# Performance work log

Measured on AMD Instinct MI355X. Metric: run time of the kernel, lower is better.

## Reference

```python
import jax, jax.numpy as jnp
import numpy as np

N_NODES = 50000


def _gcn_norm(edge_index, n):
    # add self loops, compute symmetric normalization coefficients
    src = jnp.concatenate([edge_index[0], jnp.arange(n, dtype=edge_index.dtype)])
    dst = jnp.concatenate([edge_index[1], jnp.arange(n, dtype=edge_index.dtype)])
    deg = jax.ops.segment_sum(jnp.ones_like(dst, dtype=jnp.float32), dst, num_segments=n)
    dis = jnp.where(deg > 0, jax.lax.rsqrt(jnp.maximum(deg, 1.0)), 0.0)
    norm = dis[src] * dis[dst]  # [E+n]
    return src, dst, norm


def _gcn_conv(x, W, b, src, dst, norm, n):
    xw = x @ W                      # [n, out]
    msg = xw[src] * norm[:, None]   # gather + scale
    out = jax.ops.segment_sum(msg, dst, num_segments=n)
    return out + b


def setup_inputs() -> dict:
    key = jax.random.key(0)
    ks = jax.random.split(key, 12)
    n, d, h, E, P = N_NODES, 512, 512, 400000, 200000
    sc = lambda fan_in: 1.0 / np.sqrt(fan_in)
    return {
        "x": jax.random.normal(ks[0], (n, d), dtype=jnp.float32),
        "edge_index": jax.random.randint(ks[1], (2, E), 0, n, dtype=jnp.int32),
        "edge_pairs": jax.random.randint(ks[2], (2, P), 0, n, dtype=jnp.int32),
        "W1": jax.random.uniform(ks[3], (d, h), jnp.float32, -sc(d), sc(d)),
        "b1": jnp.zeros((h,), jnp.float32),
        "W2": jax.random.uniform(ks[4], (h, h), jnp.float32, -sc(h), sc(h)),
        "b2": jnp.zeros((h,), jnp.float32),
        "lpW1": jax.random.uniform(ks[5], (2 * h, h), jnp.float32, -sc(2 * h), sc(2 * h)),
        "lpb1": jax.random.uniform(ks[6], (h,), jnp.float32, -sc(2 * h), sc(2 * h)),
        "lpW2": jax.random.uniform(ks[7], (h, 1), jnp.float32, -sc(h), sc(h)),
        "lpb2": jax.random.uniform(ks[8], (1,), jnp.float32, -sc(h), sc(h)),
    }


def reference(x, edge_index, edge_pairs, W1, b1, W2, b2, lpW1, lpb1, lpW2, lpb2):
    n = x.shape[0]
    src, dst, norm = _gcn_norm(edge_index, n)
    # encoder: GCNConv -> relu -> (dropout is identity at inference) -> GCNConv
    z = _gcn_conv(x, W1, b1, src, dst, norm, n)
    z = jax.nn.relu(z)
    z = _gcn_conv(z, W2, b2, src, dst, norm, n)
    # link predictor: gather-concat MLP
    h = jnp.concatenate([z[edge_pairs[0]], z[edge_pairs[1]]], axis=-1)  # [P, 2h]
    h = jax.nn.relu(h @ lpW1 + lpb1)
    logits = (h @ lpW2 + lpb2)[:, 0]
    return jax.nn.sigmoid(logits)
```

## Files before the change

kernel.cpp:

```cpp
#include <hip/hip_runtime.h>
#include <math.h>

#define TPB 256

typedef __attribute__((ext_vector_type(8))) short bf16x8;
typedef __attribute__((ext_vector_type(4))) float f32x4;

__device__ __forceinline__ unsigned cvt_bf(float f) {
    unsigned u = __float_as_uint(f);
    u += 0x7fffu + ((u >> 16) & 1u);
    return u >> 16;
}
__device__ __forceinline__ unsigned pack2(float a, float b) {
    return cvt_bf(a) | (cvt_bf(b) << 16);
}

__device__ __forceinline__ void gload16(const void* g, void* l) {
    __builtin_amdgcn_global_load_lds(
        (const __attribute__((address_space(1))) void*)g,
        (__attribute__((address_space(3))) void*)l, 16, 0, 0);
}


__global__ void k_hist(const int* __restrict__ dst, int* __restrict__ cnt, int E) {
    int e = blockIdx.x * TPB + threadIdx.x;
    if (e < E) atomicAdd(&cnt[dst[e]], 1);
}

__global__ __launch_bounds__(256)
void k_scan1(const int* __restrict__ cnt, int* __restrict__ incl,
             int* __restrict__ bsum, int n) {
    __shared__ int sh[256];
    const int t = threadIdx.x;
    const int i = blockIdx.x * 256 + t;
    int v = (i < n) ? cnt[i] : 0;
    sh[t] = v;
    __syncthreads();
#pragma unroll
    for (int d = 1; d < 256; d <<= 1) {
        int u = (t >= d) ? sh[t - d] : 0;
        __syncthreads();
        sh[t] += u;
        __syncthreads();
    }
    if (i < n) incl[i] = sh[t];
    if (t == 255) bsum[blockIdx.x] = sh[255];
}

__global__ __launch_bounds__(256)
void k_scan2(int* __restrict__ bsum, int* __restrict__ boff,
             int* __restrict__ row_start, int n, int nb) {
    __shared__ int sh[256];
    const int t = threadIdx.x;
    int v = (t < nb) ? bsum[t] : 0;
    sh[t] = v;
    __syncthreads();
#pragma unroll
    for (int d = 1; d < 256; d <<= 1) {
        int u = (t >= d) ? sh[t - d] : 0;
        __syncthreads();
        sh[t] += u;
        __syncthreads();
    }
    if (t < nb) boff[t] = sh[t] - v;
    if (t == nb - 1) row_start[n] = sh[t];
}

__global__ void k_scan3(const int* __restrict__ cnt, const int* __restrict__ incl,
                        const int* __restrict__ boff, int* __restrict__ row_start,
                        int* __restrict__ cursor, float* __restrict__ dis, int n) {
    int i = blockIdx.x * TPB + threadIdx.x;
    if (i >= n) return;
    int c = cnt[i];
    int ex = boff[i >> 8] + incl[i] - c;
    row_start[i] = ex;
    cursor[i] = ex;
    dis[i] = rsqrtf((float)c + 1.0f);
}

__global__ void k_fill_csr(const int* __restrict__ src, const int* __restrict__ dst,
                           const float* __restrict__ dis, int* __restrict__ cursor,
                           int* __restrict__ csr_src, float* __restrict__ csr_nrm, int E) {
    int e = blockIdx.x * TPB + threadIdx.x;
    if (e >= E) return;
    int s = src[e], d = dst[e];
    int pos = atomicAdd(&cursor[d], 1);
    csr_src[pos] = s;
    csr_nrm[pos] = dis[s] * dis[d];
}


__global__ void k_f2bf(const float* __restrict__ in, unsigned short* __restrict__ out, int total8) {
    int i = blockIdx.x * TPB + threadIdx.x;
    if (i >= total8) return;
    float4 f0 = *(const float4*)(in + (size_t)i * 8);
    float4 f1 = *(const float4*)(in + (size_t)i * 8 + 4);
    uint4 o;
    o.x = pack2(f0.x, f0.y); o.y = pack2(f0.z, f0.w);
    o.z = pack2(f1.x, f1.y); o.w = pack2(f1.z, f1.w);
    *(uint4*)(out + (size_t)i * 8) = o;
}

__global__ void k_cvtT(const float* __restrict__ in, unsigned short* __restrict__ out, int K, int N) {
    int id = blockIdx.x * TPB + threadIdx.x;
    if (id >= K * N) return;
    int k = id / N, nn = id % N;
    out[(size_t)nn * K + k] = (unsigned short)cvt_bf(in[id]);
}

__global__ void k_cvtT_lp(const float* __restrict__ in, unsigned short* __restrict__ out) {
    int id = blockIdx.x * TPB + threadIdx.x;
    if (id >= 1024 * 512) return;
    int j = id >> 9, k = id & 511;
    float v = (j < 512) ? in[(size_t)k * 512 + j] : in[(size_t)(512 + k) * 512 + (j - 512)];
    out[id] = (unsigned short)cvt_bf(v);
}

__global__ __launch_bounds__(256)
void k_bias_lp(const float* __restrict__ lpW1, const float* __restrict__ b2,
               const float* __restrict__ lpb1, float* __restrict__ bias_big) {
    const int j = blockIdx.x * 4 + (threadIdx.x >> 6);
    if (j >= 1024) return;
    const int lane = threadIdx.x & 63;
    const int col = (j < 512) ? j : (j - 512);
    const int ro = (j < 512) ? 0 : 512;
    float s = 0.f;
#pragma unroll
    for (int it = 0; it < 8; ++it) {
        int k = lane + it * 64;
        s = fmaf(b2[k], lpW1[(size_t)(ro + k) * 512 + col], s);
    }
    s += __shfl_xor(s, 1, 64);
    s += __shfl_xor(s, 2, 64);
    s += __shfl_xor(s, 4, 64);
    s += __shfl_xor(s, 8, 64);
    s += __shfl_xor(s, 16, 64);
    s += __shfl_xor(s, 32, 64);
    if (lane == 0) bias_big[j] = s + ((j < 512) ? lpb1[j] : 0.f);
}


__global__ __launch_bounds__(256)
void k_agg_bf(const unsigned short* __restrict__ xin, const int* __restrict__ row_start,
              const int* __restrict__ csr_src, const float* __restrict__ csr_nrm,
              const float* __restrict__ dis, unsigned short* __restrict__ out, int n) {
    const int v = (blockIdx.x * TPB + threadIdx.x) >> 6;
    if (v >= n) return;
    const int lane = threadIdx.x & 63;
    const uint4* base = (const uint4*)xin;

    float d = dis[v]; float d2 = d * d;
    float acc[8];
    {
        uint4 u = base[(size_t)v * 64 + lane];
        acc[0] = d2 * __uint_as_float(u.x << 16);
        acc[1] = d2 * __uint_as_float(u.x & 0xffff0000u);
        acc[2] = d2 * __uint_as_float(u.y << 16);
        acc[3] = d2 * __uint_as_float(u.y & 0xffff0000u);
        acc[4] = d2 * __uint_as_float(u.z << 16);
        acc[5] = d2 * __uint_as_float(u.z & 0xffff0000u);
        acc[6] = d2 * __uint_as_float(u.w << 16);
        acc[7] = d2 * __uint_as_float(u.w & 0xffff0000u);
    }
    const int beg = row_start[v], end = row_start[v + 1];
    for (int j = beg; j < end; ++j) {
        int s = csr_src[j];
        float r = csr_nrm[j];
        uint4 u = base[(size_t)s * 64 + lane];
        acc[0] = fmaf(__uint_as_float(u.x << 16), r, acc[0]);
        acc[1] = fmaf(__uint_as_float(u.x & 0xffff0000u), r, acc[1]);
        acc[2] = fmaf(__uint_as_float(u.y << 16), r, acc[2]);
        acc[3] = fmaf(__uint_as_float(u.y & 0xffff0000u), r, acc[3]);
        acc[4] = fmaf(__uint_as_float(u.z << 16), r, acc[4]);
        acc[5] = fmaf(__uint_as_float(u.z & 0xffff0000u), r, acc[5]);
        acc[6] = fmaf(__uint_as_float(u.w << 16), r, acc[6]);
        acc[7] = fmaf(__uint_as_float(u.w & 0xffff0000u), r, acc[7]);
    }
    uint4 o;
    o.x = pack2(acc[0], acc[1]); o.y = pack2(acc[2], acc[3]);
    o.z = pack2(acc[4], acc[5]); o.w = pack2(acc[6], acc[7]);
    ((uint4*)out)[(size_t)v * 64 + lane] = o;
}


__global__ __launch_bounds__(256)
void k_gemm_bf(const unsigned short* __restrict__ A, const unsigned short* __restrict__ Bt,
               const float* __restrict__ bias, unsigned short* __restrict__ C,
               int M, int K, int N, int do_relu, int nbx) {
    const int lin = blockIdx.x;
    const int xcd = lin & 7, seq = lin >> 3;
    const int rowt = xcd + 8 * (seq / nbx);
    const int colt = seq % nbx;
    const int m0 = rowt * 128;
    if (m0 >= M + 127) return;
    const int n0 = colt * 128;

    __shared__ __align__(16) char Asl[128 * 64];
    __shared__ __align__(16) char Bsl[128 * 64];
    const int t = threadIdx.x;
    const int wid = t >> 6, l = t & 63;
    const int wr = (wid >> 1) * 64, wc = (wid & 1) * 64;
    const int lrow = l & 15, g = l >> 4;

    const int srow = (l >> 2);
    const int cb_src = ((l & 3) * 16) ^ ((srow & 3) << 4);
    const int r0 = wid * 32 + srow, r1 = r0 + 16;
    const size_t rowA0 = (size_t)min(m0 + r0, M - 1) * K * 2;
    const size_t rowA1 = (size_t)min(m0 + r1, M - 1) * K * 2;
    const size_t rowB0 = (size_t)(n0 + r0) * K * 2;
    const size_t rowB1 = (size_t)(n0 + r1) * K * 2;
    const char* Ab = (const char*)A;
    const char* Bb = (const char*)Bt;
    char* ldsA0 = Asl + (wid * 32) * 64;
    char* ldsA1 = ldsA0 + 16 * 64;
    char* ldsB0 = Bsl + (wid * 32) * 64;
    char* ldsB1 = ldsB0 + 16 * 64;

    f32x4 acc[4][4] = {};
    for (int k0 = 0; k0 < K; k0 += 32) {
        const size_t koff = (size_t)k0 * 2 + cb_src;
        gload16(Ab + rowA0 + koff, ldsA0);
        gload16(Ab + rowA1 + koff, ldsA1);
        gload16(Bb + rowB0 + koff, ldsB0);
        gload16(Bb + rowB1 + koff, ldsB1);
        __syncthreads();
        bf16x8 af[4], bfr[4];
#pragma unroll
        for (int i = 0; i < 4; ++i)
            af[i] = *(const bf16x8*)(Asl + (wr + i * 16 + lrow) * 64 + ((g * 16) ^ ((lrow & 3) << 4)));
#pragma unroll
        for (int j = 0; j < 4; ++j)
            bfr[j] = *(const bf16x8*)(Bsl + (wc + j * 16 + lrow) * 64 + ((g * 16) ^ ((lrow & 3) << 4)));
#pragma unroll
        for (int i = 0; i < 4; ++i)
#pragma unroll
            for (int j = 0; j < 4; ++j)
                acc[i][j] = __builtin_amdgcn_mfma_f32_16x16x32_bf16(af[i], bfr[j], acc[i][j], 0, 0, 0);
        __syncthreads();
    }
    float bv[4];
#pragma unroll
    for (int j = 0; j < 4; ++j) bv[j] = bias[n0 + wc + j * 16 + lrow];
#pragma unroll
    for (int i = 0; i < 4; ++i) {
        const int rb = m0 + wr + i * 16 + g * 4;
#pragma unroll
        for (int e = 0; e < 4; ++e) {
            const int row = rb + e;
            if (row < M) {
#pragma unroll
                for (int j = 0; j < 4; ++j) {
                    float vv = acc[i][j][e] + bv[j];
                    if (do_relu) vv = fmaxf(vv, 0.f);
                    C[(size_t)row * N + n0 + wc + j * 16 + lrow] = (unsigned short)cvt_bf(vv);
                }
            }
        }
    }
}


__global__ __launch_bounds__(256)
void k_pair(const unsigned short* __restrict__ uv, const int* __restrict__ pair, int P,
            const float* __restrict__ w2, const float* __restrict__ lpb2,
            float* __restrict__ out) {
    const int idx = (blockIdx.x * TPB + threadIdx.x) >> 6;
    if (idx >= P) return;
    const int lane = threadIdx.x & 63;
    const int p0n = pair[idx], p1n = pair[P + idx];
    const uint4 a = *(const uint4*)(uv + (size_t)p0n * 1024 + lane * 8);
    const uint4 b = *(const uint4*)(uv + (size_t)p1n * 1024 + 512 + lane * 8);
    const float4 w0 = *(const float4*)(w2 + lane * 8);
    const float4 w1 = *(const float4*)(w2 + lane * 8 + 4);
    const unsigned ua[4] = {a.x, a.y, a.z, a.w};
    const unsigned ub[4] = {b.x, b.y, b.z, b.w};
    const float wv[8] = {w0.x, w0.y, w0.z, w0.w, w1.x, w1.y, w1.z, w1.w};
    float s = 0.f;
#pragma unroll
    for (int q = 0; q < 4; ++q) {
        float h0 = __uint_as_float(ua[q] << 16) + __uint_as_float(ub[q] << 16);
        float h1 = __uint_as_float(ua[q] & 0xffff0000u) + __uint_as_float(ub[q] & 0xffff0000u);
        s = fmaf(fmaxf(h0, 0.f), wv[2 * q], s);
        s = fmaf(fmaxf(h1, 0.f), wv[2 * q + 1], s);
    }
    s += __shfl_xor(s, 1, 64);
    s += __shfl_xor(s, 2, 64);
    s += __shfl_xor(s, 4, 64);
    s += __shfl_xor(s, 8, 64);
    s += __shfl_xor(s, 16, 64);
    s += __shfl_xor(s, 32, 64);
    if (lane == 0) out[idx] = 1.0f / (1.0f + expf(-(s + lpb2[0])));
}


extern "C" void kernel_launch(void* const* d_in, const int* in_sizes, int n_in,
                              void* d_out, int out_size, void* d_ws, size_t ws_size,
                              hipStream_t stream) {
    const float* x    = (const float*)d_in[0];
    const int*   ei   = (const int*)d_in[1];
    const int*   ep   = (const int*)d_in[2];
    const float* W1   = (const float*)d_in[3];
    const float* b1   = (const float*)d_in[4];
    const float* W2   = (const float*)d_in[5];
    const float* b2   = (const float*)d_in[6];
    const float* lpW1 = (const float*)d_in[7];
    const float* lpb1 = (const float*)d_in[8];
    const float* lpW2 = (const float*)d_in[9];
    const float* lpb2 = (const float*)d_in[10];

    const int n = in_sizes[0] / 512;
    const int E = in_sizes[1] / 2;
    const int P = in_sizes[2] / 2;
    const int* src = ei;
    const int* dst = ei + E;

    char* w = (char*)d_ws;
    size_t off = 0;
    auto alloc = [&](size_t bytes) {
        void* p = w + off;
        off = (off + bytes + 255) & ~(size_t)255;
        return p;
    };
    int*   cnt       = (int*)alloc((size_t)n * 4);
    int*   incl      = (int*)alloc((size_t)n * 4);
    int*   bsum      = (int*)alloc((size_t)256 * 4);
    int*   boff      = (int*)alloc((size_t)256 * 4);
    int*   row_start = (int*)alloc((size_t)(n + 1) * 4);
    int*   cursor    = (int*)alloc((size_t)n * 4);
    int*   csr_src   = (int*)alloc((size_t)E * 4);
    float* csr_nrm   = (float*)alloc((size_t)E * 4);
    float* dis       = (float*)alloc((size_t)n * 4);
    unsigned short* w1t    = (unsigned short*)alloc((size_t)512 * 512 * 2);
    unsigned short* w2bf   = (unsigned short*)alloc((size_t)512 * 512 * 2);
    unsigned short* lpw1t  = (unsigned short*)alloc((size_t)1024 * 512 * 2);
    unsigned short* wfT    = (unsigned short*)alloc((size_t)1024 * 512 * 2);
    float* bias_big  = (float*)alloc((size_t)1024 * 4);
    float* zerob     = (float*)alloc((size_t)1024 * 4);
    unsigned short* bufA = (unsigned short*)alloc((size_t)n * 512 * 2);
    unsigned short* bufB = (unsigned short*)alloc((size_t)n * 512 * 2);
    unsigned short* uv   = (unsigned short*)alloc((size_t)n * 1024 * 2);

    dim3 blk(TPB);
    const int nb_n = (n + TPB - 1) / TPB;
    const int nb_E = (E + TPB - 1) / TPB;
    const int nb_scan = (n + 255) / 256;

    hipMemsetAsync(cnt, 0, (size_t)n * 4, stream);
    hipMemsetAsync(zerob, 0, (size_t)1024 * 4, stream);
    k_hist<<<nb_E, blk, 0, stream>>>(dst, cnt, E);
    k_scan1<<<nb_scan, 256, 0, stream>>>(cnt, incl, bsum, n);
    k_scan2<<<1, 256, 0, stream>>>(bsum, boff, row_start, n, nb_scan);
    k_scan3<<<nb_n, blk, 0, stream>>>(cnt, incl, boff, row_start, cursor, dis, n);
    k_fill_csr<<<nb_E, blk, 0, stream>>>(src, dst, dis, cursor, csr_src, csr_nrm, E);

    k_f2bf<<<(n * 64 + TPB - 1) / TPB, blk, 0, stream>>>(x, bufA, n * 64);
    k_cvtT<<<(512 * 512 + TPB - 1) / TPB, blk, 0, stream>>>(W1, w1t, 512, 512);
    k_f2bf<<<(512 * 64 + TPB - 1) / TPB, blk, 0, stream>>>(W2, w2bf, 512 * 64);
    k_cvtT_lp<<<(1024 * 512 + TPB - 1) / TPB, blk, 0, stream>>>(lpW1, lpw1t);
    k_bias_lp<<<256, blk, 0, stream>>>(lpW1, b2, lpb1, bias_big);

    const int gy  = (n + 127) / 128;
    const int gy8 = ((gy + 7) / 8) * 8;
    const int agg_blocks = (n * 64 + TPB - 1) / TPB;

    k_gemm_bf<<<4 * 8, blk, 0, stream>>>(lpw1t, w2bf, zerob, wfT, 1024, 512, 512, 0, 4);

    k_agg_bf<<<agg_blocks, blk, 0, stream>>>(bufA, row_start, csr_src, csr_nrm, dis, bufB, n);
    k_gemm_bf<<<4 * gy8, blk, 0, stream>>>(bufB, w1t, b1, bufA, n, 512, 512, 1, 4);
    k_agg_bf<<<agg_blocks, blk, 0, stream>>>(bufA, row_start, csr_src, csr_nrm, dis, bufB, n);
    k_gemm_bf<<<8 * gy8, blk, 0, stream>>>(bufB, wfT, bias_big, uv, n, 512, 1024, 0, 8);

    k_pair<<<(P * 64 + TPB - 1) / TPB, blk, 0, stream>>>(uv, ep, P, lpW2, lpb2, (float*)d_out);
}
```

Baseline: 447.9 us.

## Deepen GEMM K-step, stage epilogue through LDS, unroll aggregation, use hardware bf16 pack

The GEMM now loads a 64-wide K slice per iteration into a doubled LDS buffer, which halves the number of barrier pairs per tile. Its epilogue writes results to LDS and then issues vectorized 16-byte bf16 stores instead of scattered 2-byte stores. The aggregation loop is unrolled by two so two neighbor rows are gathered in flight at once. Float-to-bf16 packing switches to the HIP intrinsic, which may map to a native convert instruction. The costs are more LDS per block, which can lower occupancy, and the LDS reuse in the epilogue relies on explicit waitcnt and scheduling barriers.

```diff
diff --git a/kernel.cpp b/kernel.cpp
--- a/kernel.cpp
+++ b/kernel.cpp
@@ -1,4 +1,5 @@
 #include <hip/hip_runtime.h>
+#include <hip/hip_bf16.h>
 #include <math.h>
 
 #define TPB 256
@@ -13,6 +14,12 @@
 }
 __device__ __forceinline__ unsigned pack2(float a, float b) {
     return cvt_bf(a) | (cvt_bf(b) << 16);
+}
+__device__ __forceinline__ unsigned pack2f(float a, float b) {
+    __hip_bfloat162 h = __float22bfloat162_rn(float2{a, b});
+    unsigned u;
+    __builtin_memcpy(&u, &h, 4);
+    return u;
 }
 
 __device__ __forceinline__ void gload16(const void* g, void* l) {
@@ -96,8 +103,8 @@
     float4 f0 = *(const float4*)(in + (size_t)i * 8);
     float4 f1 = *(const float4*)(in + (size_t)i * 8 + 4);
     uint4 o;
-    o.x = pack2(f0.x, f0.y); o.y = pack2(f0.z, f0.w);
-    o.z = pack2(f1.x, f1.y); o.w = pack2(f1.z, f1.w);
+    o.x = pack2f(f0.x, f0.y); o.y = pack2f(f0.z, f0.w);
+    o.z = pack2f(f1.x, f1.y); o.w = pack2f(f1.z, f1.w);
     *(uint4*)(out + (size_t)i * 8) = o;
 }
 
@@ -139,6 +146,17 @@
     if (lane == 0) bias_big[j] = s + ((j < 512) ? lpb1[j] : 0.f);
 }
 
+
+__device__ __forceinline__ void fma8(float* acc, uint4 u, float r) {
+    acc[0] = fmaf(__uint_as_float(u.x << 16), r, acc[0]);
+    acc[1] = fmaf(__uint_as_float(u.x & 0xffff0000u), r, acc[1]);
+    acc[2] = fmaf(__uint_as_float(u.y << 16), r, acc[2]);
+    acc[3] = fmaf(__uint_as_float(u.y & 0xffff0000u), r, acc[3]);
+    acc[4] = fmaf(__uint_as_float(u.z << 16), r, acc[4]);
+    acc[5] = fmaf(__uint_as_float(u.z & 0xffff0000u), r, acc[5]);
+    acc[6] = fmaf(__uint_as_float(u.w << 16), r, acc[6]);
+    acc[7] = fmaf(__uint_as_float(u.w & 0xffff0000u), r, acc[7]);
+}
 
 __global__ __launch_bounds__(256)
 void k_agg_bf(const unsigned short* __restrict__ xin, const int* __restrict__ row_start,
@@ -163,22 +181,22 @@
         acc[7] = d2 * __uint_as_float(u.w & 0xffff0000u);
     }
     const int beg = row_start[v], end = row_start[v + 1];
-    for (int j = beg; j < end; ++j) {
-        int s = csr_src[j];
-        float r = csr_nrm[j];
-        uint4 u = base[(size_t)s * 64 + lane];
-        acc[0] = fmaf(__uint_as_float(u.x << 16), r, acc[0]);
-        acc[1] = fmaf(__uint_as_float(u.x & 0xffff0000u), r, acc[1]);
-        acc[2] = fmaf(__uint_as_float(u.y << 16), r, acc[2]);
-        acc[3] = fmaf(__uint_as_float(u.y & 0xffff0000u), r, acc[3]);
-        acc[4] = fmaf(__uint_as_float(u.z << 16), r, acc[4]);
-        acc[5] = fmaf(__uint_as_float(u.z & 0xffff0000u), r, acc[5]);
-        acc[6] = fmaf(__uint_as_float(u.w << 16), r, acc[6]);
-        acc[7] = fmaf(__uint_as_float(u.w & 0xffff0000u), r, acc[7]);
+    int j = beg;
+    for (; j + 1 < end; j += 2) {
+        int s0 = csr_src[j], s1 = csr_src[j + 1];
+        float r0 = csr_nrm[j], r1 = csr_nrm[j + 1];
+        uint4 u0 = base[(size_t)s0 * 64 + lane];
+        uint4 u1 = base[(size_t)s1 * 64 + lane];
+        fma8(acc, u0, r0);
+        fma8(acc, u1, r1);
+    }
+    if (j < end) {
+        uint4 u = base[(size_t)csr_src[j] * 64 + lane];
+        fma8(acc, u, csr_nrm[j]);
     }
     uint4 o;
-    o.x = pack2(acc[0], acc[1]); o.y = pack2(acc[2], acc[3]);
-    o.z = pack2(acc[4], acc[5]); o.w = pack2(acc[6], acc[7]);
+    o.x = pack2f(acc[0], acc[1]); o.y = pack2f(acc[2], acc[3]);
+    o.z = pack2f(acc[4], acc[5]); o.w = pack2f(acc[6], acc[7]);
     ((uint4*)out)[(size_t)v * 64 + lane] = o;
 }
 
@@ -195,8 +213,8 @@
     if (m0 >= M + 127) return;
     const int n0 = colt * 128;
 
-    __shared__ __align__(16) char Asl[128 * 64];
-    __shared__ __align__(16) char Bsl[128 * 64];
+    __shared__ __align__(16) char Asl[2 * 128 * 64];
+    __shared__ __align__(16) char Bsl[2 * 128 * 64];
     const int t = threadIdx.x;
     const int wid = t >> 6, l = t & 63;
     const int wr = (wid >> 1) * 64, wc = (wid & 1) * 64;
@@ -215,47 +233,72 @@
     char* ldsA1 = ldsA0 + 16 * 64;
     char* ldsB0 = Bsl + (wid * 32) * 64;
     char* ldsB1 = ldsB0 + 16 * 64;
+    const int rd_off = (g * 16) ^ ((lrow & 3) << 4);
 
     f32x4 acc[4][4] = {};
-    for (int k0 = 0; k0 < K; k0 += 32) {
-        const size_t koff = (size_t)k0 * 2 + cb_src;
-        gload16(Ab + rowA0 + koff, ldsA0);
-        gload16(Ab + rowA1 + koff, ldsA1);
-        gload16(Bb + rowB0 + koff, ldsB0);
-        gload16(Bb + rowB1 + koff, ldsB1);
-        __syncthreads();
-        bf16x8 af[4], bfr[4];
-#pragma unroll
-        for (int i = 0; i < 4; ++i)
-            af[i] = *(const bf16x8*)(Asl + (wr + i * 16 + lrow) * 64 + ((g * 16) ^ ((lrow & 3) << 4)));
-#pragma unroll
-        for (int j = 0; j < 4; ++j)
-            bfr[j] = *(const bf16x8*)(Bsl + (wc + j * 16 + lrow) * 64 + ((g * 16) ^ ((lrow & 3) << 4)));
-#pragma unroll
-        for (int i = 0; i < 4; ++i)
+    for (int k0 = 0; k0 < K; k0 += 64) {
+        const size_t kf0 = (size_t)k0 * 2 + cb_src;
+        const size_t kf1 = kf0 + 64;
+        gload16(Ab + rowA0 + kf0, ldsA0);
+        gload16(Ab + rowA1 + kf0, ldsA1);
+        gload16(Ab + rowA0 + kf1, ldsA0 + 8192);
+        gload16(Ab + rowA1 + kf1, ldsA1 + 8192);
+        gload16(Bb + rowB0 + kf0, ldsB0);
+        gload16(Bb + rowB1 + kf0, ldsB1);
+        gload16(Bb + rowB0 + kf1, ldsB0 + 8192);
+        gload16(Bb + rowB1 + kf1, ldsB1 + 8192);
+        __syncthreads();
+#pragma unroll
+        for (int ks = 0; ks < 2; ++ks) {
+            bf16x8 af[4], bfr[4];
+#pragma unroll
+            for (int i = 0; i < 4; ++i)
+                af[i] = *(const bf16x8*)(Asl + ks * 8192 + (wr + i * 16 + lrow) * 64 + rd_off);
 #pragma unroll
             for (int j = 0; j < 4; ++j)
-                acc[i][j] = __builtin_amdgcn_mfma_f32_16x16x32_bf16(af[i], bfr[j], acc[i][j], 0, 0, 0);
-        __syncthreads();
-    }
+                bfr[j] = *(const bf16x8*)(Bsl + ks * 8192 + (wc + j * 16 + lrow) * 64 + rd_off);
+#pragma unroll
+            for (int i = 0; i < 4; ++i)
+#pragma unroll
+                for (int j = 0; j < 4; ++j)
+                    acc[i][j] = __builtin_amdgcn_mfma_f32_16x16x32_bf16(af[i], bfr[j], acc[i][j], 0, 0, 0);
+        }
+        __syncthreads();
+    }
+
     float bv[4];
 #pragma unroll
     for (int j = 0; j < 4; ++j) bv[j] = bias[n0 + wc + j * 16 + lrow];
+    float* lws = (float*)Asl + wid * 1024;
+    const int rrow = l >> 2, rcol = (l & 3) * 16;
 #pragma unroll
     for (int i = 0; i < 4; ++i) {
-        const int rb = m0 + wr + i * 16 + g * 4;
-#pragma unroll
-        for (int e = 0; e < 4; ++e) {
-            const int row = rb + e;
-            if (row < M) {
-#pragma unroll
-                for (int j = 0; j < 4; ++j) {
-                    float vv = acc[i][j][e] + bv[j];
-                    if (do_relu) vv = fmaxf(vv, 0.f);
-                    C[(size_t)row * N + n0 + wc + j * 16 + lrow] = (unsigned short)cvt_bf(vv);
-                }
+#pragma unroll
+        for (int e = 0; e < 4; ++e)
+#pragma unroll
+            for (int j = 0; j < 4; ++j) {
+                float vv = acc[i][j][e] + bv[j];
+                if (do_relu) vv = fmaxf(vv, 0.f);
+                lws[(g * 4 + e) * 64 + j * 16 + lrow] = vv;
             }
+        asm volatile("s_waitcnt lgkmcnt(0)" ::: "memory");
+        __builtin_amdgcn_sched_barrier(0);
+        const int grow = m0 + wr + i * 16 + rrow;
+        float4 f0 = *(const float4*)&lws[rrow * 64 + rcol];
+        float4 f1 = *(const float4*)&lws[rrow * 64 + rcol + 4];
+        float4 f2 = *(const float4*)&lws[rrow * 64 + rcol + 8];
+        float4 f3 = *(const float4*)&lws[rrow * 64 + rcol + 12];
+        if (grow < M) {
+            uint4 o0, o1;
+            o0.x = pack2f(f0.x, f0.y); o0.y = pack2f(f0.z, f0.w);
+            o0.z = pack2f(f1.x, f1.y); o0.w = pack2f(f1.z, f1.w);
+            o1.x = pack2f(f2.x, f2.y); o1.y = pack2f(f2.z, f2.w);
+            o1.z = pack2f(f3.x, f3.y); o1.w = pack2f(f3.z, f3.w);
+            *(uint4*)(C + (size_t)grow * N + n0 + wc + rcol)     = o0;
+            *(uint4*)(C + (size_t)grow * N + n0 + wc + rcol + 8) = o1;
         }
+        asm volatile("s_waitcnt lgkmcnt(0)" ::: "memory");
+        __builtin_amdgcn_sched_barrier(0);
     }
 }
 
@@ -345,8 +388,8 @@
     const int nb_E = (E + TPB - 1) / TPB;
     const int nb_scan = (n + 255) / 256;
 
-    hipMemsetAsync(cnt, 0, (size_t)n * 4, stream);
-    hipMemsetAsync(zerob, 0, (size_t)1024 * 4, stream);
+    (void)hipMemsetAsync(cnt, 0, (size_t)n * 4, stream);
+    (void)hipMemsetAsync(zerob, 0, (size_t)1024 * 4, stream);
     k_hist<<<nb_E, blk, 0, stream>>>(dst, cnt, E);
     k_scan1<<<nb_scan, 256, 0, stream>>>(cnt, incl, bsum, n);
     k_scan2<<<1, 256, 0, stream>>>(bsum, boff, row_start, n, nb_scan);
```

After: 442.3 us. About the same (-1.3%).
